# Kernel optimization log

Hardware: AMD Instinct MI355X
Metric: run time of the kernel (lower is better)

## Reference

```python
import jax, jax.numpy as jnp
import numpy as np

B, IN, HID, H = 8192, 1024, 2048, 8
UP = 2 * IN          # input_size * proj_factor
HS = HID // H        # head size = 256
EPS = 1e-5


def _blockdiag(x, w, b):
    # x: [B, UP] -> chunk into H blocks of UP//H, per-block linear to HID//H
    xb = x.reshape(B, H, UP // H)
    y = jnp.einsum('bhi,hio->bho', xb, w)
    return y.reshape(B, HID) + b


def setup_inputs() -> dict:
    key = jax.random.key(0)
    ks = jax.random.split(key, 20)
    rn = lambda k, s: jax.random.normal(k, s, jnp.float32)
    p = lambda k, *s: rn(k, s) * 0.02
    return dict(
        x=rn(ks[0], (B, IN)),
        h_prev=rn(ks[1], (B, HID)), c_prev=rn(ks[2], (B, HID)),
        n_prev=rn(ks[3], (B, HID)), m_prev=rn(ks[4], (B, HID)),
        ln_g=jnp.ones(IN), ln_b=jnp.zeros(IN),
        w_ul=p(ks[5], IN, UP), b_ul=jnp.zeros(UP),
        w_ur=p(ks[6], IN, HID), b_ur=jnp.zeros(HID),
        conv_w=p(ks[7], 4), conv_b=jnp.zeros(()),
        w_skip=p(ks[8], UP, HID), b_skip=jnp.zeros(HID),
        w_q=p(ks[9], H, UP // H, HID // H), b_q=jnp.zeros(HID),
        w_k=p(ks[10], H, UP // H, HID // H), b_k=jnp.zeros(HID),
        w_v=p(ks[11], H, UP // H, HID // H), b_v=jnp.zeros(HID),
        w_i=p(ks[12], UP, HID), b_i=jnp.zeros(HID),
        w_f=p(ks[13], UP, HID), b_f=jnp.zeros(HID),
        w_o=p(ks[14], UP, HID), b_o=jnp.zeros(HID),
        gn_g=jnp.ones(HID), gn_b=jnp.zeros(HID),
        w_down=p(ks[15], HID, IN), b_down=jnp.zeros(IN),
    )


def reference(x, h_prev, c_prev, n_prev, m_prev, ln_g, ln_b,
              w_ul, b_ul, w_ur, b_ur, conv_w, conv_b, w_skip, b_skip,
              w_q, b_q, w_k, b_k, w_v, b_v, w_i, b_i, w_f, b_f, w_o, b_o,
              gn_g, gn_b, w_down, b_down):
    # LayerNorm over features
    mu = x.mean(-1, keepdims=True)
    var = x.var(-1, keepdims=True)
    xn = (x - mu) * jax.lax.rsqrt(var + EPS) * ln_g + ln_b

    xul = xn @ w_ul + b_ul          # [B, UP]
    xur = xn @ w_ur + b_ur          # [B, HID]

    # causal conv1d (kernel 4, 1 channel) along the feature axis, left-pad 3
    xp = jnp.pad(xul, ((0, 0), (3, 0)))
    xc = conv_b + sum(conv_w[j] * xp[:, j:j + UP] for j in range(4))
    xc = jax.nn.silu(xc)            # [B, UP]

    x_skip = xc @ w_skip + b_skip

    q = _blockdiag(xc, w_q, b_q)
    k = _blockdiag(xc, w_k, b_k) / np.sqrt(HS).astype(np.float32)
    v = _blockdiag(xul, w_v, b_v)

    i_t = xc @ w_i + b_i
    f_t = xc @ w_f + b_f
    o = jax.nn.sigmoid(xul @ w_o + b_o)

    m_t = jnp.maximum(f_t + m_prev, i_t)
    i = jnp.exp(i_t - m_t)
    f = jnp.exp(f_t + m_prev - m_t)
    c_t = f * c_prev + i * (v * k)
    n_t = f * n_prev + i * k

    denom = jnp.max(jnp.abs(n_t.T @ q), axis=1)     # [HID]
    h_t = o * (c_t * q) / denom

    # GroupNorm on (N, C), groups = H
    hg = h_t.reshape(B, H, HID // H)
    gm = hg.mean(-1, keepdims=True)
    gv = hg.var(-1, keepdims=True)
    hn = ((hg - gm) * jax.lax.rsqrt(gv + EPS)).reshape(B, HID) * gn_g + gn_b

    out = (hn + x_skip) * jax.nn.silu(xur)
    return out @ w_down + b_down + x, h_t, c_t, n_t, m_t
```

## Files before the change

kernel.cpp:

```cpp
#include <hip/hip_runtime.h>
#include <stdint.h>

#define B_    8192
#define IN_   1024
#define HID_  2048
#define UP_   2048
#define H_    8
#define HS_   256
#define EPS_  1e-5f

typedef __bf16 bf16x8 __attribute__((ext_vector_type(8)));
typedef float f32x4 __attribute__((ext_vector_type(4)));
typedef unsigned short u16x4 __attribute__((ext_vector_type(4)));
typedef unsigned short u16x8 __attribute__((ext_vector_type(8)));

__device__ __forceinline__ unsigned short f2bf(float f) {
  union { float f; unsigned int u; } v; v.f = f;
  unsigned int u = v.u;
  unsigned int r = (u + 0x7fffu + ((u >> 16) & 1u)) >> 16;
  return (unsigned short)r;
}
__device__ __forceinline__ float bf2f(unsigned short h) {
  union { unsigned int u; float f; } v; v.u = ((unsigned int)h) << 16;
  return v.f;
}

__device__ __forceinline__ void gload_lds16(const void* g, void* l) {
  auto gp = reinterpret_cast<const uint32_t __attribute__((address_space(1)))*>(
      reinterpret_cast<uintptr_t>(g));
  auto lp = reinterpret_cast<uint32_t __attribute__((address_space(3)))*>(
      reinterpret_cast<uintptr_t>(l));
  __builtin_amdgcn_global_load_lds(gp, lp, 16, 0, 0);
}

template <typename OutT, bool HAS_ADD>
__global__ __launch_bounds__(512, 2) void gemm8p(
    const unsigned short* __restrict__ A, int lda, int a_zoff,
    const unsigned short* __restrict__ W, int ldw, int w_zoff,
    const float* __restrict__ bias, const float* __restrict__ bias2,
    int bias_zoff,
    OutT* __restrict__ C, OutT* __restrict__ C2, int ldc, int c_zoff,
    int c_split,
    const float* __restrict__ ADD, float scale, float scale2, int K)
{
  __shared__ char lds[131072];
  const int z = blockIdx.z;
  A += (size_t)z * a_zoff;
  W += (size_t)z * w_zoff;
  if (bias) bias += (size_t)z * bias_zoff;
  if (bias2) bias2 += (size_t)z * bias_zoff;

  const int nwg = gridDim.x * gridDim.y;
  const int orig = blockIdx.y * gridDim.x + blockIdx.x;
  const int q8 = nwg >> 3, r8 = nwg & 7;
  const int xcd = orig & 7, xi = orig >> 3;
  const int wg = (xcd < r8 ? xcd * (q8 + 1) : r8 * (q8 + 1) + (xcd - r8) * q8) + xi;
  const int bx = wg % gridDim.x, by = wg / gridDim.x;

  const int t = threadIdx.x;
  const int lane = t & 63, wave = t >> 6;
  const int wr = wave >> 2, wc = wave & 3;
  const int l15 = lane & 15, l4 = lane >> 4;
  const int row0 = by * 256, col0 = bx * 256;

  const int lrow = lane >> 3;
  const int lslot = (lane & 7) ^ lrow;
  const size_t aLane = (size_t)lrow * lda * 2 + (size_t)lslot * 16;
  const size_t wLane = (size_t)lrow * ldw * 2 + (size_t)lslot * 16;
  const char* Abase = (const char*)A;
  const char* Wbase = (const char*)W;

  const int aRdBase = (wr * 128 + l15) * 128 + (((l4) ^ (l15 & 7)) * 16);
  const int bRdBase = (wc * 64 + l15) * 128 + (((l4) ^ (l15 & 7)) * 16);

  auto issueA = [&](int buf, int half, int tile) {
#pragma unroll
    for (int j = 0; j < 2; ++j) {
      const int rbase = half * 128 + j * 64 + wave * 8;
      gload_lds16(Abase + (size_t)(row0 + rbase) * (lda * 2) + (size_t)tile * 128 + aLane,
                  lds + buf * 65536 + rbase * 128 + lane * 16);
    }
  };
  auto issueB = [&](int buf, int half, int tile) {
#pragma unroll
    for (int j = 0; j < 2; ++j) {
      const int rbase = half * 128 + j * 64 + wave * 8;
      gload_lds16(Wbase + (size_t)(col0 + rbase) * (ldw * 2) + (size_t)tile * 128 + wLane,
                  lds + buf * 65536 + 32768 + rbase * 128 + lane * 16);
    }
  };

  f32x4 acc[8][4] = {};
  const int NT = K >> 6;

  issueA(0, 0, 0); issueA(0, 1, 0);
  issueB(0, 0, 0); issueB(0, 1, 0);
  issueB(1, 0, 1); issueB(1, 1, 1);
  asm volatile("s_waitcnt vmcnt(4)" ::: "memory");
  __builtin_amdgcn_s_barrier();
  __builtin_amdgcn_sched_barrier(0);

  for (int T = 0; T < NT; ++T) {
    const int buf = T & 1;
    const char* ldsA = lds + buf * 65536;
    const char* ldsB = ldsA + 32768;
    bf16x8 bfr[4][2];
#pragma unroll
    for (int q = 0; q < 4; ++q) {
      if (q == 0) {
#pragma unroll
        for (int ni = 0; ni < 4; ++ni) {
          bfr[ni][0] = *(const bf16x8*)(ldsB + (bRdBase + ni * 2048));
          bfr[ni][1] = *(const bf16x8*)(ldsB + ((bRdBase + ni * 2048) ^ 64));
        }
      }
      bf16x8 af[2][2];
#pragma unroll
      for (int m2 = 0; m2 < 2; ++m2) {
        const int mi = q * 2 + m2;
        af[m2][0] = *(const bf16x8*)(ldsA + (aRdBase + mi * 2048));
        af[m2][1] = *(const bf16x8*)(ldsA + ((aRdBase + mi * 2048) ^ 64));
      }
      if (q == 0 && T + 1 < NT) issueA(buf ^ 1, 0, T + 1);
      if (q == 1 && T + 1 < NT) issueA(buf ^ 1, 1, T + 1);
      if (q == 2 && T + 2 < NT) issueB(buf, 0, T + 2);
      if (q == 3 && T + 2 < NT) issueB(buf, 1, T + 2);
      if (q == 0) asm volatile("s_waitcnt lgkmcnt(8)" ::: "memory");
      __builtin_amdgcn_s_barrier();
      asm volatile("s_waitcnt lgkmcnt(0)" ::: "memory");
      __builtin_amdgcn_sched_barrier(0);
      __builtin_amdgcn_s_setprio(1);
#pragma unroll
      for (int kq = 0; kq < 2; ++kq)
#pragma unroll
        for (int m2 = 0; m2 < 2; ++m2)
#pragma unroll
          for (int ni = 0; ni < 4; ++ni)
            acc[q * 2 + m2][ni] = __builtin_amdgcn_mfma_f32_16x16x32_bf16(
                af[m2][kq], bfr[ni][kq], acc[q * 2 + m2][ni], 0, 0, 0);
      __builtin_amdgcn_s_setprio(0);
      if (q == 3) {
        if (T + 2 < NT) asm volatile("s_waitcnt vmcnt(4)" ::: "memory");
        else            asm volatile("s_waitcnt vmcnt(0)" ::: "memory");
      }
      __builtin_amdgcn_s_barrier();
      __builtin_amdgcn_sched_barrier(0);
    }
  }

  const float* bp = bias;
  OutT* Cp = C;
  int cbase = col0;
  float sc = scale;
  if (col0 >= c_split) { bp = bias2; Cp = C2; cbase = col0 - c_split; sc = scale2; }
#pragma unroll
  for (int mi = 0; mi < 8; ++mi) {
#pragma unroll
    for (int ni = 0; ni < 4; ++ni) {
#pragma unroll
      for (int r = 0; r < 4; ++r) {
        const int m = row0 + wr * 128 + mi * 16 + l4 * 4 + r;
        const int n = wc * 64 + ni * 16 + l15;
        float v = acc[mi][ni][r];
        if (bp) v += bp[cbase + n];
        v *= sc;
        const size_t ci = (size_t)m * ldc + (size_t)z * c_zoff + cbase + n;
        if constexpr (HAS_ADD) v += ADD[ci];
        if constexpr (sizeof(OutT) == 2) Cp[ci] = (OutT)f2bf(v);
        else Cp[ci] = v;
      }
    }
  }
}

__global__ __launch_bounds__(256) void denom_reduce(
    const float* __restrict__ part, float* __restrict__ denom)
{
  const int m = blockIdx.x, t = threadIdx.x;
  const size_t P = (size_t)HID_ * HID_;
  float v = 0.f;
  for (int n = t; n < HID_; n += 256) {
    const size_t o = (size_t)m * HID_ + n;
    float s = part[o] + part[P + o] + part[2 * P + o] + part[3 * P + o];
    v = fmaxf(v, fabsf(s));
  }
#pragma unroll
  for (int off = 1; off < 64; off <<= 1) v = fmaxf(v, __shfl_xor(v, off, 64));
  __shared__ float red[4];
  if ((t & 63) == 0) red[t >> 6] = v;
  __syncthreads();
  if (t == 0) denom[m] = fmaxf(fmaxf(red[0], red[1]), fmaxf(red[2], red[3]));
}

template <typename InT>
__global__ __launch_bounds__(256) void transpose_bf(
    const InT* __restrict__ in, unsigned short* __restrict__ out, int R, int C,
    int izoff, int ozoff)
{
  __shared__ float tile[32][33];
  in += (size_t)blockIdx.z * izoff;
  out += (size_t)blockIdx.z * ozoff;
  const int cb = blockIdx.x * 32, rb = blockIdx.y * 32;
  const int tx = threadIdx.x, ty = threadIdx.y;
  for (int i = ty; i < 32; i += 8) {
    InT v = in[(size_t)(rb + i) * C + cb + tx];
    float f;
    if constexpr (sizeof(InT) == 2) f = bf2f((unsigned short)v);
    else f = (float)v;
    tile[i][tx] = f;
  }
  __syncthreads();
  for (int i = ty; i < 32; i += 8)
    out[(size_t)(cb + i) * R + rb + tx] = f2bf(tile[tx][i]);
}

__global__ __launch_bounds__(256) void ln_kernel(
    const float* __restrict__ x, const float* __restrict__ g,
    const float* __restrict__ b, unsigned short* __restrict__ xn)
{
  const int brow = blockIdx.x, t = threadIdx.x;
  const int lane = t & 63, wave = t >> 6;
  const float* xr = x + (size_t)brow * IN_;
  f32x4 v = *(const f32x4*)(xr + t * 4);
  float s = v[0] + v[1] + v[2] + v[3];
  float q = v[0]*v[0] + v[1]*v[1] + v[2]*v[2] + v[3]*v[3];
#pragma unroll
  for (int off = 32; off; off >>= 1) {
    s += __shfl_xor(s, off, 64);
    q += __shfl_xor(q, off, 64);
  }
  __shared__ float ss[4], sq[4];
  if (lane == 0) { ss[wave] = s; sq[wave] = q; }
  __syncthreads();
  s = ss[0] + ss[1] + ss[2] + ss[3];
  q = sq[0] + sq[1] + sq[2] + sq[3];
  const float mean = s * (1.f / IN_);
  const float var = q * (1.f / IN_) - mean * mean;
  const float rs = rsqrtf(var + EPS_);
  u16x4 o;
#pragma unroll
  for (int e = 0; e < 4; ++e) {
    const int j = t * 4 + e;
    o[e] = f2bf((v[e] - mean) * rs * g[j] + b[j]);
  }
  *(u16x4*)(xn + (size_t)brow * IN_ + t * 4) = o;
}

__global__ __launch_bounds__(256) void conv_kernel(
    const unsigned short* __restrict__ xul, const float* __restrict__ cw,
    const float* __restrict__ cb, unsigned short* __restrict__ xc)
{
  const int brow = blockIdx.x, t = threadIdx.x;
  const size_t base = (size_t)brow * UP_;
  const int j0 = t * 8;
  float xv[11];
#pragma unroll
  for (int e = 0; e < 11; ++e) {
    const int j = j0 + e - 3;
    xv[e] = (j >= 0) ? bf2f(xul[base + j]) : 0.f;
  }
  const float w0 = cw[0], w1 = cw[1], w2 = cw[2], w3 = cw[3], bb = cb[0];
  u16x8 o;
#pragma unroll
  for (int e = 0; e < 8; ++e) {
    float sv = bb + w0 * xv[e] + w1 * xv[e + 1] + w2 * xv[e + 2] + w3 * xv[e + 3];
    o[e] = f2bf(sv / (1.f + expf(-sv)));
  }
  *(u16x8*)(xc + base + j0) = o;
}

__global__ __launch_bounds__(256) void gates_kernel(
    const unsigned short* __restrict__ sif,
    const unsigned short* __restrict__ kb, const unsigned short* __restrict__ vb,
    const float* __restrict__ mprev, const float* __restrict__ cprev,
    const float* __restrict__ nprev,
    float* __restrict__ mo, float* __restrict__ co, float* __restrict__ no,
    unsigned short* __restrict__ nT)
{
  __shared__ unsigned short nt_t[64][72];
  const int t = threadIdx.x;
  const int r = t >> 2, cq = t & 3;
  const int row = blockIdx.y * 64 + r;
  const int colb = blockIdx.x * 64 + cq * 16;
  const size_t hidb = (size_t)row * HID_ + colb;
  const size_t sifb = (size_t)row * 6144 + colb;
#pragma unroll
  for (int e4 = 0; e4 < 4; ++e4) {
    const int c4 = e4 * 4;
    f32x4 mp = *(const f32x4*)(mprev + hidb + c4);
    f32x4 cp = *(const f32x4*)(cprev + hidb + c4);
    f32x4 np = *(const f32x4*)(nprev + hidb + c4);
    u16x4 iv = *(const u16x4*)(sif + sifb + 2048 + c4);
    u16x4 fv = *(const u16x4*)(sif + sifb + 4096 + c4);
    u16x4 kv = *(const u16x4*)(kb + hidb + c4);
    u16x4 vv = *(const u16x4*)(vb + hidb + c4);
    f32x4 mo4, co4, no4;
#pragma unroll
    for (int e = 0; e < 4; ++e) {
      const float ft = bf2f(fv[e]) + mp[e];
      const float it = bf2f(iv[e]);
      const float mt = fmaxf(ft, it);
      const float ie = expf(it - mt);
      const float fe = expf(ft - mt);
      const float k = bf2f(kv[e]), v = bf2f(vv[e]);
      mo4[e] = mt;
      co4[e] = fe * cp[e] + ie * (v * k);
      no4[e] = fe * np[e] + ie * k;
      nt_t[r][cq * 16 + c4 + e] = f2bf(no4[e]);
    }
    *(f32x4*)(mo + hidb + c4) = mo4;
    *(f32x4*)(co + hidb + c4) = co4;
    *(f32x4*)(no + hidb + c4) = no4;
  }
  __syncthreads();
  const int cT = t >> 2, sq = t & 3;
  u16x8 o0, o1;
#pragma unroll
  for (int e = 0; e < 8; ++e) {
    o0[e] = nt_t[sq * 16 + e][cT];
    o1[e] = nt_t[sq * 16 + 8 + e][cT];
  }
  const size_t ob = (size_t)(blockIdx.x * 64 + cT) * B_ + blockIdx.y * 64 + sq * 16;
  *(u16x8*)(nT + ob) = o0;
  *(u16x8*)(nT + ob + 8) = o1;
}

__global__ __launch_bounds__(256) void hgn_kernel(
    const float* __restrict__ ct, const unsigned short* __restrict__ olin,
    const unsigned short* __restrict__ qb, const float* __restrict__ denom,
    const unsigned short* __restrict__ sif, const unsigned short* __restrict__ xurb,
    const float* __restrict__ gng, const float* __restrict__ gnb,
    float* __restrict__ ho, unsigned short* __restrict__ pre)
{
  const int brow = blockIdx.x, t = threadIdx.x;
  const size_t base = (size_t)brow * HID_ + t * 8;
  u16x8 ov = *(const u16x8*)(olin + base);
  u16x8 qv = *(const u16x8*)(qb + base);
  f32x4 c0 = *(const f32x4*)(ct + base);
  f32x4 c1 = *(const f32x4*)(ct + base + 4);
  float h[8];
  float s = 0.f, sq = 0.f;
#pragma unroll
  for (int e = 0; e < 8; ++e) {
    const float o = 1.f / (1.f + expf(-bf2f(ov[e])));
    const float cv = (e < 4) ? c0[e] : c1[e - 4];
    const float hv = o * cv * bf2f(qv[e]) / denom[t * 8 + e];
    h[e] = hv; s += hv; sq += hv * hv;
  }
#pragma unroll
  for (int e = 0; e < 8; ++e) ho[base + e] = h[e];
#pragma unroll
  for (int off = 1; off < 32; off <<= 1) {
    s += __shfl_xor(s, off, 64);
    sq += __shfl_xor(sq, off, 64);
  }
  const float mean = s * (1.f / HS_);
  const float var = sq * (1.f / HS_) - mean * mean;
  const float rs = rsqrtf(var + EPS_);
  u16x8 sv = *(const u16x8*)(sif + (size_t)brow * 6144 + t * 8);
  u16x8 xv = *(const u16x8*)(xurb + base);
  u16x8 pv;
#pragma unroll
  for (int e = 0; e < 8; ++e) {
    const int j = t * 8 + e;
    const float hn = (h[e] - mean) * rs * gng[j] + gnb[j];
    const float xr = bf2f(xv[e]);
    const float sil = xr / (1.f + expf(-xr));
    pv[e] = f2bf((hn + bf2f(sv[e])) * sil);
  }
  *(u16x8*)(pre + base) = pv;
}

extern "C" void kernel_launch(void* const* d_in, const int* in_sizes, int n_in,
                              void* d_out, int out_size, void* d_ws, size_t ws_size,
                              hipStream_t stream)
{
  const float* x      = (const float*)d_in[0];
  const float* c_prev = (const float*)d_in[2];
  const float* n_prev = (const float*)d_in[3];
  const float* m_prev = (const float*)d_in[4];
  const float* ln_g   = (const float*)d_in[5];
  const float* ln_b   = (const float*)d_in[6];
  const float* w_ul   = (const float*)d_in[7];
  const float* b_ul   = (const float*)d_in[8];
  const float* w_ur   = (const float*)d_in[9];
  const float* b_ur   = (const float*)d_in[10];
  const float* conv_w = (const float*)d_in[11];
  const float* conv_b = (const float*)d_in[12];
  const float* w_skip = (const float*)d_in[13];
  const float* b_skip = (const float*)d_in[14];
  const float* w_q    = (const float*)d_in[15];
  const float* b_q    = (const float*)d_in[16];
  const float* w_k    = (const float*)d_in[17];
  const float* b_k    = (const float*)d_in[18];
  const float* w_v    = (const float*)d_in[19];
  const float* b_v    = (const float*)d_in[20];
  const float* w_i    = (const float*)d_in[21];
  const float* b_i    = (const float*)d_in[22];
  const float* w_f    = (const float*)d_in[23];
  const float* b_f    = (const float*)d_in[24];
  const float* w_o    = (const float*)d_in[25];
  const float* b_o    = (const float*)d_in[26];
  const float* gn_g   = (const float*)d_in[27];
  const float* gn_b   = (const float*)d_in[28];
  const float* w_down = (const float*)d_in[29];
  const float* b_down = (const float*)d_in[30];

  float* out_p = (float*)d_out;
  float* h_p = out_p + (size_t)B_ * IN_;
  float* c_p = h_p + (size_t)B_ * HID_;
  float* n_p = c_p + (size_t)B_ * HID_;
  float* m_p = n_p + (size_t)B_ * HID_;

  char* ws = (char*)d_ws;
  size_t off = 0;
  auto alloc = [&](size_t n) -> void* {
    void* p = ws + off;
    off += (n + 255) & ~(size_t)255;
    return p;
  };

  const size_t BH2 = (size_t)B_ * HID_ * 2;

  unsigned short* xn_bf   = (unsigned short*)alloc((size_t)B_ * IN_ * 2);
  unsigned short* xul_bf  = (unsigned short*)alloc(BH2);
  unsigned short* xur_bf  = (unsigned short*)alloc(BH2);
  unsigned short* xc_bf   = (unsigned short*)alloc(BH2);
  unsigned short* sif_bf  = (unsigned short*)alloc((size_t)B_ * 6144 * 2);
  unsigned short* q_bf    = (unsigned short*)alloc(BH2);
  unsigned short* k_bf    = (unsigned short*)alloc(BH2);
  unsigned short* v_bf    = (unsigned short*)alloc(BH2);
  unsigned short* olin_bf = (unsigned short*)alloc(BH2);
  unsigned short* qT_bf   = (unsigned short*)alloc(BH2);
  unsigned short* nT_bf   = (unsigned short*)alloc(BH2);
  unsigned short* pre_bf  = (unsigned short*)alloc(BH2);
  float* denom = (float*)alloc(HID_ * sizeof(float));
  float* part  = (float*)alloc((size_t)4 * HID_ * HID_ * sizeof(float));
  float* b_sif = (float*)alloc(6144 * sizeof(float));
  unsigned short* wt_ulur = (unsigned short*)alloc((size_t)4096 * IN_ * 2);
  unsigned short* wt_sif  = (unsigned short*)alloc((size_t)6144 * UP_ * 2);
  unsigned short* wt_qk   = (unsigned short*)alloc((size_t)H_ * 512 * HS_ * 2);
  unsigned short* wt_v    = (unsigned short*)alloc((size_t)H_ * HS_ * HS_ * 2);
  unsigned short* wt_o    = (unsigned short*)alloc((size_t)UP_ * HID_ * 2);
  unsigned short* wt_down = (unsigned short*)alloc((size_t)HID_ * IN_ * 2);

  if (off > ws_size) return;

  const dim3 tb32(32, 8);
  const int NOSPLIT = 1 << 30;

  hipMemcpyAsync(b_sif, b_skip, 2048 * 4, hipMemcpyDeviceToDevice, stream);
  hipMemcpyAsync(b_sif + 2048, b_i, 2048 * 4, hipMemcpyDeviceToDevice, stream);
  hipMemcpyAsync(b_sif + 4096, b_f, 2048 * 4, hipMemcpyDeviceToDevice, stream);

  transpose_bf<float><<<dim3(64, 32, 1), tb32, 0, stream>>>(w_ul, wt_ulur, 1024, 2048, 0, 0);
  transpose_bf<float><<<dim3(64, 32, 1), tb32, 0, stream>>>(w_ur, wt_ulur + (size_t)2048 * 1024, 1024, 2048, 0, 0);
  transpose_bf<float><<<dim3(64, 64, 1), tb32, 0, stream>>>(w_skip, wt_sif, 2048, 2048, 0, 0);
  transpose_bf<float><<<dim3(64, 64, 1), tb32, 0, stream>>>(w_i, wt_sif + (size_t)2048 * 2048, 2048, 2048, 0, 0);
  transpose_bf<float><<<dim3(64, 64, 1), tb32, 0, stream>>>(w_f, wt_sif + (size_t)4096 * 2048, 2048, 2048, 0, 0);
  transpose_bf<float><<<dim3(8, 8, 8), tb32, 0, stream>>>(w_q, wt_qk, 256, 256, 65536, 131072);
  transpose_bf<float><<<dim3(8, 8, 8), tb32, 0, stream>>>(w_k, wt_qk + 65536, 256, 256, 65536, 131072);
  transpose_bf<float><<<dim3(8, 8, 8), tb32, 0, stream>>>(w_v, wt_v, 256, 256, 65536, 65536);
  transpose_bf<float><<<dim3(64, 64, 1), tb32, 0, stream>>>(w_o, wt_o, 2048, 2048, 0, 0);
  transpose_bf<float><<<dim3(32, 64, 1), tb32, 0, stream>>>(w_down, wt_down, 2048, 1024, 0, 0);

  ln_kernel<<<B_, 256, 0, stream>>>(x, ln_g, ln_b, xn_bf);

  gemm8p<unsigned short, false><<<dim3(16, 32, 1), 512, 0, stream>>>(
      xn_bf, IN_, 0, wt_ulur, IN_, 0, b_ul, b_ur, 0,
      xul_bf, xur_bf, HID_, 0, 2048, nullptr, 1.f, 1.f, IN_);

  conv_kernel<<<B_, 256, 0, stream>>>(xul_bf, conv_w, conv_b, xc_bf);

  gemm8p<unsigned short, false><<<dim3(24, 32, 1), 512, 0, stream>>>(
      xc_bf, UP_, 0, wt_sif, UP_, 0, b_sif, nullptr, 0,
      sif_bf, sif_bf, 6144, 0, NOSPLIT, nullptr, 1.f, 1.f, UP_);

  gemm8p<unsigned short, false><<<dim3(2, 32, 8), 512, 0, stream>>>(
      xc_bf, UP_, HS_, wt_qk, HS_, 512 * HS_, b_q, b_k, HS_,
      q_bf, k_bf, HID_, HS_, 256, nullptr, 1.f, 0.0625f, HS_);

  gemm8p<unsigned short, false><<<dim3(1, 32, 8), 512, 0, stream>>>(
      xul_bf, UP_, HS_, wt_v, HS_, HS_ * HS_, b_v, nullptr, HS_,
      v_bf, v_bf, HID_, HS_, NOSPLIT, nullptr, 1.f, 1.f, HS_);

  gemm8p<unsigned short, false><<<dim3(8, 32, 1), 512, 0, stream>>>(
      xul_bf, UP_, 0, wt_o, UP_, 0, b_o, nullptr, 0,
      olin_bf, olin_bf, HID_, 0, NOSPLIT, nullptr, 1.f, 1.f, UP_);

  gates_kernel<<<dim3(HID_ / 64, B_ / 64, 1), 256, 0, stream>>>(
      sif_bf, k_bf, v_bf, m_prev, c_prev, n_prev, m_p, c_p, n_p, nT_bf);

  transpose_bf<unsigned short><<<dim3(64, 256, 1), tb32, 0, stream>>>(
      q_bf, qT_bf, B_, HID_, 0, 0);

  gemm8p<float, false><<<dim3(8, 8, 4), 512, 0, stream>>>(
      nT_bf, B_, B_ / 4, qT_bf, B_, B_ / 4, nullptr, nullptr, 0,
      part, part, HID_, HID_ * HID_, NOSPLIT, nullptr, 1.f, 1.f, B_ / 4);
  denom_reduce<<<HID_, 256, 0, stream>>>(part, denom);

  hgn_kernel<<<B_, 256, 0, stream>>>(
      c_p, olin_bf, q_bf, denom, sif_bf, xur_bf, gn_g, gn_b, h_p, pre_bf);

  gemm8p<float, true><<<dim3(4, 32, 1), 512, 0, stream>>>(
      pre_bf, UP_, 0, wt_down, UP_, 0, b_down, nullptr, 0,
      out_p, out_p, IN_, 0, NOSPLIT, x, 1.f, 1.f, UP_);
}
```

Measured before the change: 1.076 ms.

## Triple-buffer A tiles in GEMM and split-K the down projection

The GEMM kernel now keeps three LDS buffers for A and two for B (160KB LDS), so A tiles are prefetched two iterations ahead rather than one, giving global loads more time to land. The wait counts are adjusted to match. Separately, the final down-projection GEMM, which launched only 128 workgroups, is split along K into two halves. Each half writes a partial sum, and a new elementwise kernel adds the partials, the bias and the residual. The larger LDS footprint may limit occupancy to one workgroup per CU instead of the two the launch bounds request, and the split-K path adds an extra partial-buffer write and read.

Result: faster. 1.005 ms (-6.6%).

```diff
diff --git a/kernel.cpp b/kernel.cpp
--- a/kernel.cpp
+++ b/kernel.cpp
@@ -43,7 +43,7 @@
     int c_split,
     const float* __restrict__ ADD, float scale, float scale2, int K)
 {
-  __shared__ char lds[131072];
+  __shared__ char lds[163840];
   const int z = blockIdx.z;
   A += (size_t)z * a_zoff;
   W += (size_t)z * w_zoff;
@@ -73,20 +73,20 @@
   const int aRdBase = (wr * 128 + l15) * 128 + (((l4) ^ (l15 & 7)) * 16);
   const int bRdBase = (wc * 64 + l15) * 128 + (((l4) ^ (l15 & 7)) * 16);
 
-  auto issueA = [&](int buf, int half, int tile) {
+  auto issueA = [&](int abuf, int half, int tile) {
 #pragma unroll
     for (int j = 0; j < 2; ++j) {
       const int rbase = half * 128 + j * 64 + wave * 8;
       gload_lds16(Abase + (size_t)(row0 + rbase) * (lda * 2) + (size_t)tile * 128 + aLane,
-                  lds + buf * 65536 + rbase * 128 + lane * 16);
+                  lds + abuf * 32768 + rbase * 128 + lane * 16);
     }
   };
-  auto issueB = [&](int buf, int half, int tile) {
+  auto issueB = [&](int bbuf, int half, int tile) {
 #pragma unroll
     for (int j = 0; j < 2; ++j) {
       const int rbase = half * 128 + j * 64 + wave * 8;
       gload_lds16(Wbase + (size_t)(col0 + rbase) * (ldw * 2) + (size_t)tile * 128 + wLane,
-                  lds + buf * 65536 + 32768 + rbase * 128 + lane * 16);
+                  lds + 98304 + bbuf * 32768 + rbase * 128 + lane * 16);
     }
   };
 
@@ -95,15 +95,21 @@
 
   issueA(0, 0, 0); issueA(0, 1, 0);
   issueB(0, 0, 0); issueB(0, 1, 0);
-  issueB(1, 0, 1); issueB(1, 1, 1);
-  asm volatile("s_waitcnt vmcnt(4)" ::: "memory");
+  if (NT > 1) {
+    issueA(1, 0, 1); issueA(1, 1, 1);
+    issueB(1, 0, 1); issueB(1, 1, 1);
+    asm volatile("s_waitcnt vmcnt(8)" ::: "memory");
+  } else {
+    asm volatile("s_waitcnt vmcnt(0)" ::: "memory");
+  }
   __builtin_amdgcn_s_barrier();
   __builtin_amdgcn_sched_barrier(0);
 
   for (int T = 0; T < NT; ++T) {
-    const int buf = T & 1;
-    const char* ldsA = lds + buf * 65536;
-    const char* ldsB = ldsA + 32768;
+    const char* ldsA = lds + (T % 3) * 32768;
+    const char* ldsB = lds + 98304 + (T & 1) * 32768;
+    const int abufN = (T + 2) % 3;
+    const int bbufN = T & 1;
     bf16x8 bfr[4][2];
 #pragma unroll
     for (int q = 0; q < 4; ++q) {
@@ -121,10 +127,10 @@
         af[m2][0] = *(const bf16x8*)(ldsA + (aRdBase + mi * 2048));
         af[m2][1] = *(const bf16x8*)(ldsA + ((aRdBase + mi * 2048) ^ 64));
       }
-      if (q == 0 && T + 1 < NT) issueA(buf ^ 1, 0, T + 1);
-      if (q == 1 && T + 1 < NT) issueA(buf ^ 1, 1, T + 1);
-      if (q == 2 && T + 2 < NT) issueB(buf, 0, T + 2);
-      if (q == 3 && T + 2 < NT) issueB(buf, 1, T + 2);
+      if (q == 0 && T + 2 < NT) issueA(abufN, 0, T + 2);
+      if (q == 1 && T + 2 < NT) issueA(abufN, 1, T + 2);
+      if (q == 2 && T + 2 < NT) issueB(bbufN, 0, T + 2);
+      if (q == 3 && T + 2 < NT) issueB(bbufN, 1, T + 2);
       if (q == 0) asm volatile("s_waitcnt lgkmcnt(8)" ::: "memory");
       __builtin_amdgcn_s_barrier();
       asm volatile("s_waitcnt lgkmcnt(0)" ::: "memory");
@@ -140,7 +146,7 @@
                 af[m2][kq], bfr[ni][kq], acc[q * 2 + m2][ni], 0, 0, 0);
       __builtin_amdgcn_s_setprio(0);
       if (q == 3) {
-        if (T + 2 < NT) asm volatile("s_waitcnt vmcnt(4)" ::: "memory");
+        if (T + 2 < NT) asm volatile("s_waitcnt vmcnt(8)" ::: "memory");
         else            asm volatile("s_waitcnt vmcnt(0)" ::: "memory");
       }
       __builtin_amdgcn_s_barrier();
@@ -190,6 +196,23 @@
   if ((t & 63) == 0) red[t >> 6] = v;
   __syncthreads();
   if (t == 0) denom[m] = fmaxf(fmaxf(red[0], red[1]), fmaxf(red[2], red[3]));
+}
+
+__global__ __launch_bounds__(256) void down_reduce(
+    const float* __restrict__ part, const float* __restrict__ x,
+    const float* __restrict__ bias, float* __restrict__ out)
+{
+  const size_t idx = ((size_t)blockIdx.x * 256 + threadIdx.x) * 4;
+  const size_t P = (size_t)B_ * IN_;
+  f32x4 a = *(const f32x4*)(part + idx);
+  f32x4 b = *(const f32x4*)(part + P + idx);
+  f32x4 xv = *(const f32x4*)(x + idx);
+  const int j = (int)(idx & (IN_ - 1));
+  f32x4 bv = *(const f32x4*)(bias + j);
+  f32x4 o;
+#pragma unroll
+  for (int e = 0; e < 4; ++e) o[e] = a[e] + b[e] + bv[e] + xv[e];
+  *(f32x4*)(out + idx) = o;
 }
 
 template <typename InT>
@@ -502,7 +525,8 @@
   hgn_kernel<<<B_, 256, 0, stream>>>(
       c_p, olin_bf, q_bf, denom, sif_bf, xur_bf, gn_g, gn_b, h_p, pre_bf);
 
-  gemm8p<float, true><<<dim3(4, 32, 1), 512, 0, stream>>>(
-      pre_bf, UP_, 0, wt_down, UP_, 0, b_down, nullptr, 0,
-      out_p, out_p, IN_, 0, NOSPLIT, x, 1.f, 1.f, UP_);
-}
+  gemm8p<float, false><<<dim3(4, 32, 2), 512, 0, stream>>>(
+      pre_bf, UP_, 1024, wt_down, UP_, 1024, nullptr, nullptr, 0,
+      part, part, IN_, B_ * IN_, NOSPLIT, nullptr, 1.f, 1.f, 1024);
+  down_reduce<<<(B_ * IN_ / 4) / 256, 256, 0, stream>>>(part, x, b_down, out_p);
+}
```
